# Optimization experiments

Hardware: AMD Instinct MI355X
Metric: run time of the kernel (lower is better)

Reference implementation:

```python
import jax, jax.numpy as jnp
import numpy as np

DIM = 1024
SRC_DIM = 1152
NUM_HEADS = 16
HEAD_DIM = DIM // NUM_HEADS  # 64
ROPE_BASE = 10000.0


def rope_tables(seq_len, head_dim):
    # matches RotaryPositionEmbedding: inv_freq over even indices, emb = cat([freqs, freqs])
    inv_freq = 1.0 / (ROPE_BASE ** (jnp.arange(0, head_dim, 2, dtype=jnp.float32) / head_dim))
    t = jnp.arange(seq_len, dtype=jnp.float32)
    freqs = t[:, None] * inv_freq[None, :]          # (L, D/2)
    emb = jnp.concatenate([freqs, freqs], axis=-1)  # (L, D)
    return jnp.cos(emb), jnp.sin(emb)


def rotate_half(x):
    # interleaved rotation as in the torch code
    x1 = x[..., ::2]
    x2 = x[..., 1::2]
    return jnp.stack((-x2, x1), axis=-1).reshape(x.shape)


def apply_rope(t, cos, sin):
    # t: (B, H, L, D); cos/sin: (L, D)
    return t * cos[None, None] + rotate_half(t) * sin[None, None]


def setup_inputs() -> dict:
    key = jax.random.key(0)
    ks = jax.random.split(key, 10)
    B, T, K = 2, 2048, 2048
    s_q = 1.0 / np.sqrt(DIM)
    s_kv = 1.0 / np.sqrt(SRC_DIM)
    return {
        "x": jax.random.normal(ks[0], (B, T, DIM), jnp.float32),
        "context": jax.random.normal(ks[1], (B, K, SRC_DIM), jnp.float32),
        "Wq": jax.random.normal(ks[2], (DIM, DIM), jnp.float32) * s_q,
        "bq": jnp.zeros((DIM,), jnp.float32),
        "Wk": jax.random.normal(ks[3], (DIM, SRC_DIM), jnp.float32) * s_kv,
        "bk": jnp.zeros((DIM,), jnp.float32),
        "Wv": jax.random.normal(ks[4], (DIM, SRC_DIM), jnp.float32) * s_kv,
        "bv": jnp.zeros((DIM,), jnp.float32),
        "Wo": jax.random.normal(ks[5], (DIM, DIM), jnp.float32) * s_q,
        "bo": jnp.zeros((DIM,), jnp.float32),
    }


def reference(x, context, Wq, bq, Wk, bk, Wv, bv, Wo, bo):
    B, T, C = x.shape
    K = context.shape[1]
    H, D = NUM_HEADS, HEAD_DIM

    q = x @ Wq.T + bq                 # (B, T, C)
    k = context @ Wk.T + bk           # (B, K, C)
    v = context @ Wv.T + bv           # (B, K, C)

    q = q.reshape(B, T, H, D).transpose(0, 2, 1, 3)  # (B, H, T, D)
    k = k.reshape(B, K, H, D).transpose(0, 2, 1, 3)  # (B, H, K, D)
    v = v.reshape(B, K, H, D).transpose(0, 2, 1, 3)

    cos_q, sin_q = rope_tables(T, D)
    cos_k, sin_k = rope_tables(K, D)
    q = apply_rope(q, cos_q, sin_q)
    k = apply_rope(k, cos_k, sin_k)

    scale = 1.0 / np.sqrt(D).astype(np.float32)
    scores = jnp.einsum('bhtd,bhkd->bhtk', q, k) * scale  # (B, H, T, K)
    weights = jax.nn.softmax(scores, axis=-1)
    out = jnp.einsum('bhtk,bhkd->bhtd', weights, v)        # (B, H, T, D)
    out = out.transpose(0, 2, 1, 3).reshape(B, T, C)
    return out @ Wo.T + bo
```

## Files before the change

### kernel.cpp

```cpp
#include <hip/hip_runtime.h>
#include <hip/hip_bf16.h>
#include <stdint.h>

typedef unsigned short u16;
typedef __attribute__((ext_vector_type(8))) short bf16x8;
typedef __attribute__((ext_vector_type(8))) unsigned short u16x8;
typedef __attribute__((ext_vector_type(4))) float f32x4;

#define BM 128
#define BN 128
#define BK 32
#define QBK 64
#define QSCALE 0.18033688f

__device__ __forceinline__ u16 f2bf(float f) {
    union { float f; uint32_t u; } v; v.f = f;
    uint32_t r = v.u + 0x7FFFu + ((v.u >> 16) & 1u);
    return (u16)(r >> 16);
}

__device__ __forceinline__ uint32_t cvt_pk_bf16(float lo, float hi) {
    uint32_t r;
    asm("v_cvt_pk_bf16_f32 %0, %1, %2" : "=v"(r) : "v"(lo), "v"(hi));
    return r;
}

__device__ __forceinline__ float fexp2(float x) {
    float r;
    asm volatile("v_exp_f32 %0, %1\n\ts_nop 0" : "=v"(r) : "v"(x));
    return r;
}

__device__ __forceinline__ void gload_lds16(const void* g, void* l) {
    __builtin_amdgcn_global_load_lds(
        (const __attribute__((address_space(1))) void*)(g),
        (__attribute__((address_space(3))) void*)(l),
        16, 0, 0);
}

__global__ void prep_kernel(const float* __restrict__ x, const float* __restrict__ ctx,
                            const float* __restrict__ Wq, const float* __restrict__ Wk,
                            const float* __restrict__ Wv, const float* __restrict__ Wo,
                            u16* __restrict__ xb, u16* __restrict__ cb,
                            u16* __restrict__ wqb, u16* __restrict__ wkb,
                            u16* __restrict__ wvb, u16* __restrict__ wob,
                            float2* __restrict__ cs) {
    int t = blockIdx.x * 256 + threadIdx.x;
    if (t < 3342336) {
        const float* src; u16* dst; int base;
        if      (t < 1048576) { src = x;   dst = xb;  base = 0; }
        else if (t < 2228224) { src = ctx; dst = cb;  base = 1048576; }
        else if (t < 2490368) { src = Wq;  dst = wqb; base = 2228224; }
        else if (t < 2785280) { src = Wk;  dst = wkb; base = 2490368; }
        else if (t < 3080192) { src = Wv;  dst = wvb; base = 2785280; }
        else                  { src = Wo;  dst = wob; base = 3080192; }
        int i = (t - base) * 4;
        float4 v = *reinterpret_cast<const float4*>(src + i);
        ushort4 o = { f2bf(v.x), f2bf(v.y), f2bf(v.z), f2bf(v.w) };
        *reinterpret_cast<ushort4*>(dst + i) = o;
    } else {
        int idx = t - 3342336;
        int tt = idx >> 5, j = idx & 31;
        float invf = 1.0f / powf(10000.0f, (float)(2 * j) / 64.0f);
        float ang = (float)tt * invf;
        cs[idx] = make_float2(cosf(ang), sinf(ang));
    }
}

__global__ __launch_bounds__(256, 3)
void qkv_gemm(const u16* __restrict__ xb, const u16* __restrict__ cb,
              const u16* __restrict__ wqb, const u16* __restrict__ wkb,
              const u16* __restrict__ wvb,
              const float* __restrict__ bq, const float* __restrict__ bk,
              const float* __restrict__ bv,
              u16* __restrict__ qo, u16* __restrict__ ko, u16* __restrict__ vo,
              const float2* __restrict__ cs)
{
    __shared__ __align__(16) u16 As[BM * QBK];
    __shared__ __align__(16) u16 Bs[BN * QBK];
    const int bid = blockIdx.x;
    const int wg = (bid & 7) * 96 + (bid >> 3);
    const int seg = wg >> 8, inner = wg & 255;
    const u16* A; const u16* Bm; const float* bias; u16* C;
    int N, K, mbase, nbase, rope, brow;
    float oscale;
    if (seg == 0)      { A = xb;  Bm = wqb; bias = bq; C = qo; N = 1024; K = 1024; rope = 1; brow = 0; oscale = QSCALE; nbase = (inner & 7) * BN;  mbase = (inner >> 3) * BM; }
    else if (seg == 1) { A = cb;  Bm = wkb; bias = bk; C = ko; N = 1024; K = 1152; rope = 1; brow = 0; oscale = 1.0f;   nbase = (inner & 7) * BN;  mbase = (inner >> 3) * BM; }
    else               { A = wvb; Bm = cb;  bias = bv; C = vo; N = 4096; K = 1152; rope = 0; brow = 1; oscale = 1.0f;   nbase = (inner & 31) * BN; mbase = (inner >> 5) * BM; }

    const int tid = threadIdx.x;
    const int wid = tid >> 6, lane = tid & 63;
    const int wr = wid >> 1, wc = wid & 1;
    const int l15 = lane & 15, l4 = lane >> 4;
    const int r8 = lane >> 3;
    const int cp = lane & 7;
    const int cl = cp ^ r8;

    f32x4 acc[4][4];
#pragma unroll
    for (int i = 0; i < 4; i++)
#pragma unroll
        for (int j = 0; j < 4; j++) acc[i][j] = (f32x4){0.f, 0.f, 0.f, 0.f};

    for (int k0 = 0; k0 < K; k0 += QBK) {
#pragma unroll
        for (int q = 0; q < 4; ++q) {
            int sg = wid * 4 + q;
            int row = sg * 8 + r8;
            gload_lds16(A  + (size_t)(mbase + row) * K + k0 + cl * 8, (void*)(As + sg * 512));
            gload_lds16(Bm + (size_t)(nbase + row) * K + k0 + cl * 8, (void*)(Bs + sg * 512));
        }
        __syncthreads();
        bf16x8 af[2][4], bfv[2][4];
#pragma unroll
        for (int kk = 0; kk < 2; kk++) {
#pragma unroll
            for (int i = 0; i < 4; i++) {
                int r = wr * 64 + i * 16 + l15;
                af[kk][i] = *(const bf16x8*)(As + r * 64 + (((kk * 4 + l4) ^ (r & 7)) * 8));
            }
#pragma unroll
            for (int j = 0; j < 4; j++) {
                int r = wc * 64 + j * 16 + l15;
                bfv[kk][j] = *(const bf16x8*)(Bs + r * 64 + (((kk * 4 + l4) ^ (r & 7)) * 8));
            }
        }
        __builtin_amdgcn_s_setprio(1);
#pragma unroll
        for (int kk = 0; kk < 2; kk++)
#pragma unroll
            for (int i = 0; i < 4; i++)
#pragma unroll
                for (int j = 0; j < 4; j++)
                    acc[i][j] = __builtin_amdgcn_mfma_f32_16x16x32_bf16(af[kk][i], bfv[kk][j], acc[i][j], 0, 0, 0);
        __builtin_amdgcn_s_setprio(0);
        __syncthreads();
    }

#pragma unroll
    for (int i = 0; i < 4; i++) {
#pragma unroll
        for (int j = 0; j < 4; j++) {
#pragma unroll
            for (int r = 0; r < 4; r++) {
                int row = mbase + wr * 64 + i * 16 + l4 * 4 + r;
                int col = nbase + wc * 64 + j * 16 + l15;
                float v = acc[i][j][r] + (brow ? bias[row] : bias[col]);
                if (rope) {
                    float part = __shfl_xor(v, 1);
                    float2 c2 = cs[(row & 2047) * 32 + (col & 31)];
                    v = v * c2.x + ((col & 1) ? part * c2.y : -part * c2.y);
                    v *= oscale;
                }
                C[(size_t)row * N + col] = f2bf(v);
            }
        }
    }
}

__global__ __launch_bounds__(256, 2)
void gemm_out(const u16* __restrict__ A, const u16* __restrict__ B,
              const float* __restrict__ bias, float* __restrict__ C,
              int M, int N, int K)
{
    __shared__ __align__(16) u16 As[BM * QBK];
    __shared__ __align__(16) u16 Bs[64 * QBK];
    const int tid = threadIdx.x;
    const int wid = tid >> 6, lane = tid & 63;
    const int wr = wid >> 1, wc = wid & 1;
    const int l15 = lane & 15, l4 = lane >> 4;
    const int mbase = blockIdx.y * BM, nbase = blockIdx.x * 64;
    const int r8 = lane >> 3;
    const int cp = lane & 7;
    const int cl = cp ^ r8;

    f32x4 acc[4][2];
#pragma unroll
    for (int i = 0; i < 4; i++)
#pragma unroll
        for (int j = 0; j < 2; j++) acc[i][j] = (f32x4){0.f, 0.f, 0.f, 0.f};

    for (int k0 = 0; k0 < K; k0 += QBK) {
#pragma unroll
        for (int q = 0; q < 4; ++q) {
            int sg = wid * 4 + q;
            int row = sg * 8 + r8;
            gload_lds16(A + (size_t)(mbase + row) * K + k0 + cl * 8, (void*)(As + sg * 512));
        }
        {
            int sg = wid * 2 + (lane >> 5);
        }
#pragma unroll
        for (int q = 0; q < 2; ++q) {
            int sg = wid * 2 + q;
            int row = sg * 8 + r8;
            gload_lds16(B + (size_t)(nbase + row) * K + k0 + cl * 8, (void*)(Bs + sg * 512));
        }
        __syncthreads();
        bf16x8 af[2][4], bfv[2][2];
#pragma unroll
        for (int kk = 0; kk < 2; kk++) {
#pragma unroll
            for (int i = 0; i < 4; i++) {
                int r = wr * 64 + i * 16 + l15;
                af[kk][i] = *(const bf16x8*)(As + r * 64 + (((kk * 4 + l4) ^ (r & 7)) * 8));
            }
#pragma unroll
            for (int j = 0; j < 2; j++) {
                int r = wc * 32 + j * 16 + l15;
                bfv[kk][j] = *(const bf16x8*)(Bs + r * 64 + (((kk * 4 + l4) ^ (r & 7)) * 8));
            }
        }
        __builtin_amdgcn_s_setprio(1);
#pragma unroll
        for (int kk = 0; kk < 2; kk++)
#pragma unroll
            for (int i = 0; i < 4; i++)
#pragma unroll
                for (int j = 0; j < 2; j++)
                    acc[i][j] = __builtin_amdgcn_mfma_f32_16x16x32_bf16(af[kk][i], bfv[kk][j], acc[i][j], 0, 0, 0);
        __builtin_amdgcn_s_setprio(0);
        __syncthreads();
    }

#pragma unroll
    for (int i = 0; i < 4; i++)
#pragma unroll
        for (int j = 0; j < 2; j++)
#pragma unroll
            for (int r = 0; r < 4; r++) {
                int row = mbase + wr * 64 + i * 16 + l4 * 4 + r;
                int col = nbase + wc * 32 + j * 16 + l15;
                C[(size_t)row * N + col] = acc[i][j][r] + bias[col];
            }
}

__device__ __forceinline__ int invrow(int R) {
    return 32 * (R >> 5) + 8 * ((R >> 2) & 3) + 4 * ((R >> 4) & 1) + (R & 3);
}

__global__ __launch_bounds__(512, 4)
void attn_kernel(const u16* __restrict__ Qb, const u16* __restrict__ Kb,
                 const u16* __restrict__ VT, u16* __restrict__ Ob)
{
    const int qt = blockIdx.x;
    const int bh = blockIdx.y;
    const int b = bh >> 4, h = bh & 15;
    __shared__ __align__(16) u16 Ks[2][4096];
    __shared__ __align__(16) u16 Vs[2][4096];
    const int tid = threadIdx.x, wv = tid >> 6, lane = tid & 63;
    const int l15 = lane & 15, l4 = lane >> 4;

    const int r8 = lane >> 3;
    const int cp = lane & 7;
    const int cl = cp ^ r8;
    const int RK = wv * 8 + r8;
    const u16* ksrc = Kb + (size_t)(b * 2048 + invrow(RK)) * 1024 + h * 64 + cl * 8;
    const u16* vsrc = VT + (size_t)(h * 64 + RK) * 4096 + b * 2048 + cl * 8;

    const u16* qrow = Qb + (size_t)(b * 2048 + qt * 128 + wv * 16 + l15) * 1024 + h * 64;
    bf16x8 qf0 = *(const bf16x8*)(qrow + l4 * 8);
    bf16x8 qf1 = *(const bf16x8*)(qrow + 32 + l4 * 8);

    const int swz = l15 & 7;
    const int q0o = (l4 ^ swz) * 8;
    const int q1o = ((4 + l4) ^ swz) * 8;

    f32x4 accO[4];
    float denom = 0.f;
#pragma unroll
    for (int i = 0; i < 4; i++) accO[i] = (f32x4){0.f, 0.f, 0.f, 0.f};

    auto stageK = [&](int bs, int kt) {
        gload_lds16(ksrc + (size_t)kt * 65536, (void*)&Ks[bs][wv * 512]);
    };
    auto stageV = [&](int bs, int kt) {
        gload_lds16(vsrc + kt * 64, (void*)&Vs[bs][wv * 512]);
    };

    stageK(0, 0);
    __syncthreads();

    f32x4 sA[4], sB[4];

    auto finish_tile = [&](f32x4 (&sold)[4], int vbuf) {
        float p[4][4];
        float rs = 0.f;
#pragma unroll
        for (int j = 0; j < 4; j++)
#pragma unroll
            for (int r = 0; r < 4; r++) {
                p[j][r] = fexp2(sold[j][r]);
                rs += p[j][r];
            }
        rs += __shfl_xor(rs, 16);
        rs += __shfl_xor(rs, 32);
        denom += rs;
        union { uint32_t u[4]; bf16x8 v; } B0u, B1u;
        B0u.u[0] = cvt_pk_bf16(p[0][0], p[0][1]);
        B0u.u[1] = cvt_pk_bf16(p[0][2], p[0][3]);
        B0u.u[2] = cvt_pk_bf16(p[1][0], p[1][1]);
        B0u.u[3] = cvt_pk_bf16(p[1][2], p[1][3]);
        B1u.u[0] = cvt_pk_bf16(p[2][0], p[2][1]);
        B1u.u[1] = cvt_pk_bf16(p[2][2], p[2][3]);
        B1u.u[2] = cvt_pk_bf16(p[3][0], p[3][1]);
        B1u.u[3] = cvt_pk_bf16(p[3][2], p[3][3]);
        __builtin_amdgcn_s_setprio(1);
#pragma unroll
        for (int i = 0; i < 4; i++) {
            const u16* vp = &Vs[vbuf][(i * 16 + l15) * 64];
            bf16x8 v0 = *(const bf16x8*)(vp + q0o);
            bf16x8 v1 = *(const bf16x8*)(vp + q1o);
            accO[i] = __builtin_amdgcn_mfma_f32_16x16x32_bf16(v0, B0u.v, accO[i], 0, 0, 0);
            accO[i] = __builtin_amdgcn_mfma_f32_16x16x32_bf16(v1, B1u.v, accO[i], 0, 0, 0);
        }
        __builtin_amdgcn_s_setprio(0);
    };

    auto body = [&](int kt, f32x4 (&snew)[4], f32x4 (&sold)[4]) {
        const int kb = kt & 1;
#pragma unroll
        for (int j = 0; j < 4; j++) snew[j] = (f32x4){0.f, 0.f, 0.f, 0.f};
        __builtin_amdgcn_s_setprio(1);
#pragma unroll
        for (int j = 0; j < 4; j++) {
            const u16* rp = &Ks[kb][(j * 16 + l15) * 64];
            bf16x8 a0 = *(const bf16x8*)(rp + q0o);
            bf16x8 a1 = *(const bf16x8*)(rp + q1o);
            snew[j] = __builtin_amdgcn_mfma_f32_16x16x32_bf16(a0, qf0, snew[j], 0, 0, 0);
            snew[j] = __builtin_amdgcn_mfma_f32_16x16x32_bf16(a1, qf1, snew[j], 0, 0, 0);
        }
        __builtin_amdgcn_s_setprio(0);
        if (kt < 31) stageK(kb ^ 1, kt + 1);
        stageV(kb ^ 1, kt);
        if (kt > 0) finish_tile(sold, kb);
        __syncthreads();
    };

    for (int kt2 = 0; kt2 < 32; kt2 += 2) {
        body(kt2, sA, sB);
        body(kt2 + 1, sB, sA);
    }
    finish_tile(sB, 0);

    float rd = 1.0f / denom;
    u16* orow = Ob + (size_t)(b * 2048 + qt * 128 + wv * 16 + l15) * 1024 + h * 64;
#pragma unroll
    for (int i = 0; i < 4; i++) {
        uint2 st;
        st.x = cvt_pk_bf16(accO[i][0] * rd, accO[i][1] * rd);
        st.y = cvt_pk_bf16(accO[i][2] * rd, accO[i][3] * rd);
        *(uint2*)(orow + i * 16 + l4 * 4) = st;
    }
}

extern "C" void kernel_launch(void* const* d_in, const int* in_sizes, int n_in,
                              void* d_out, int out_size, void* d_ws, size_t ws_size,
                              hipStream_t stream) {
    const float* x   = (const float*)d_in[0];
    const float* ctx = (const float*)d_in[1];
    const float* Wq  = (const float*)d_in[2];
    const float* bq  = (const float*)d_in[3];
    const float* Wk  = (const float*)d_in[4];
    const float* bk  = (const float*)d_in[5];
    const float* Wv  = (const float*)d_in[6];
    const float* bv  = (const float*)d_in[7];
    const float* Wo  = (const float*)d_in[8];
    const float* bo  = (const float*)d_in[9];
    float* out = (float*)d_out;

    char* ws = (char*)d_ws;
    size_t off = 0;
    auto alloc = [&](size_t bytes) { void* p = ws + off; off += (bytes + 255) & ~255ULL; return p; };
    u16* x_bf  = (u16*)alloc(4096ULL * 1024 * 2);
    u16* c_bf  = (u16*)alloc(4096ULL * 1152 * 2);
    u16* wq_bf = (u16*)alloc(1024ULL * 1024 * 2);
    u16* wk_bf = (u16*)alloc(1024ULL * 1152 * 2);
    u16* wv_bf = (u16*)alloc(1024ULL * 1152 * 2);
    u16* wo_bf = (u16*)alloc(1024ULL * 1024 * 2);
    float2* cs = (float2*)alloc(2048ULL * 32 * 8);
    u16* q_bf  = (u16*)alloc(4096ULL * 1024 * 2);
    u16* k_bf  = (u16*)alloc(4096ULL * 1024 * 2);
    u16* vT    = (u16*)alloc(1024ULL * 4096 * 2);
    u16* a_bf  = (u16*)alloc(4096ULL * 1024 * 2);

    prep_kernel<<<13312, 256, 0, stream>>>(x, ctx, Wq, Wk, Wv, Wo,
                                           x_bf, c_bf, wq_bf, wk_bf, wv_bf, wo_bf, cs);
    qkv_gemm<<<768, 256, 0, stream>>>(x_bf, c_bf, wq_bf, wk_bf, wv_bf,
                                      bq, bk, bv, q_bf, k_bf, vT, cs);
    attn_kernel<<<dim3(16, 32), 512, 0, stream>>>(q_bf, k_bf, vT, a_bf);
    gemm_out<<<dim3(16, 32), 256, 0, stream>>>(a_bf, wo_bf, bo, out, 4096, 1024, 1024);
}
```

Measured before the change: 125.9 us.

## Process two KV tiles per barrier with four-slot K/V LDS ring

The attention loop now handles two key tiles per iteration, with K and V staged into a four-slot LDS ring instead of a double buffer. This halves the number of __syncthreads barriers and gives more independent MFMA work between them. In exchange LDS use doubles, launch bounds drop from 4 to 2 blocks per CU, and more score registers are live, so occupancy falls. A dead leftover block in the projection GEMM is also removed.

```diff
diff --git a/kernel.cpp b/kernel.cpp
--- a/kernel.cpp
+++ b/kernel.cpp
@@ -187,9 +187,6 @@
             int row = sg * 8 + r8;
             gload_lds16(A + (size_t)(mbase + row) * K + k0 + cl * 8, (void*)(As + sg * 512));
         }
-        {
-            int sg = wid * 2 + (lane >> 5);
-        }
 #pragma unroll
         for (int q = 0; q < 2; ++q) {
             int sg = wid * 2 + q;
@@ -239,15 +236,15 @@
     return 32 * (R >> 5) + 8 * ((R >> 2) & 3) + 4 * ((R >> 4) & 1) + (R & 3);
 }
 
-__global__ __launch_bounds__(512, 4)
+__global__ __launch_bounds__(512, 2)
 void attn_kernel(const u16* __restrict__ Qb, const u16* __restrict__ Kb,
                  const u16* __restrict__ VT, u16* __restrict__ Ob)
 {
     const int qt = blockIdx.x;
     const int bh = blockIdx.y;
     const int b = bh >> 4, h = bh & 15;
-    __shared__ __align__(16) u16 Ks[2][4096];
-    __shared__ __align__(16) u16 Vs[2][4096];
+    __shared__ __align__(16) u16 Ks[4][4096];
+    __shared__ __align__(16) u16 Vs[4][4096];
     const int tid = threadIdx.x, wv = tid >> 6, lane = tid & 63;
     const int l15 = lane & 15, l4 = lane >> 4;
 
@@ -271,19 +268,36 @@
 #pragma unroll
     for (int i = 0; i < 4; i++) accO[i] = (f32x4){0.f, 0.f, 0.f, 0.f};
 
-    auto stageK = [&](int bs, int kt) {
-        gload_lds16(ksrc + (size_t)kt * 65536, (void*)&Ks[bs][wv * 512]);
+    auto stageK = [&](int slot, int kt) {
+        gload_lds16(ksrc + (size_t)kt * 65536, (void*)&Ks[slot][wv * 512]);
     };
-    auto stageV = [&](int bs, int kt) {
-        gload_lds16(vsrc + kt * 64, (void*)&Vs[bs][wv * 512]);
+    auto stageV = [&](int slot, int kt) {
+        gload_lds16(vsrc + kt * 64, (void*)&Vs[slot][wv * 512]);
     };
 
     stageK(0, 0);
+    stageK(1, 1);
     __syncthreads();
 
-    f32x4 sA[4], sB[4];
-
-    auto finish_tile = [&](f32x4 (&sold)[4], int vbuf) {
+    f32x4 sA0[4], sA1[4], sB0[4], sB1[4];
+
+    auto qk = [&](int kt, f32x4 (&s)[4]) {
+#pragma unroll
+        for (int j = 0; j < 4; j++) s[j] = (f32x4){0.f, 0.f, 0.f, 0.f};
+        const int slot = kt & 3;
+        __builtin_amdgcn_s_setprio(1);
+#pragma unroll
+        for (int j = 0; j < 4; j++) {
+            const u16* rp = &Ks[slot][(j * 16 + l15) * 64];
+            bf16x8 a0 = *(const bf16x8*)(rp + q0o);
+            bf16x8 a1 = *(const bf16x8*)(rp + q1o);
+            s[j] = __builtin_amdgcn_mfma_f32_16x16x32_bf16(a0, qf0, s[j], 0, 0, 0);
+            s[j] = __builtin_amdgcn_mfma_f32_16x16x32_bf16(a1, qf1, s[j], 0, 0, 0);
+        }
+        __builtin_amdgcn_s_setprio(0);
+    };
+
+    auto finish_tile = [&](f32x4 (&sold)[4], int vslot) {
         float p[4][4];
         float rs = 0.f;
 #pragma unroll
@@ -308,7 +322,7 @@
         __builtin_amdgcn_s_setprio(1);
 #pragma unroll
         for (int i = 0; i < 4; i++) {
-            const u16* vp = &Vs[vbuf][(i * 16 + l15) * 64];
+            const u16* vp = &Vs[vslot][(i * 16 + l15) * 64];
             bf16x8 v0 = *(const bf16x8*)(vp + q0o);
             bf16x8 v1 = *(const bf16x8*)(vp + q1o);
             accO[i] = __builtin_amdgcn_mfma_f32_16x16x32_bf16(v0, B0u.v, accO[i], 0, 0, 0);
@@ -317,31 +331,28 @@
         __builtin_amdgcn_s_setprio(0);
     };
 
-    auto body = [&](int kt, f32x4 (&snew)[4], f32x4 (&sold)[4]) {
-        const int kb = kt & 1;
-#pragma unroll
-        for (int j = 0; j < 4; j++) snew[j] = (f32x4){0.f, 0.f, 0.f, 0.f};
-        __builtin_amdgcn_s_setprio(1);
-#pragma unroll
-        for (int j = 0; j < 4; j++) {
-            const u16* rp = &Ks[kb][(j * 16 + l15) * 64];
-            bf16x8 a0 = *(const bf16x8*)(rp + q0o);
-            bf16x8 a1 = *(const bf16x8*)(rp + q1o);
-            snew[j] = __builtin_amdgcn_mfma_f32_16x16x32_bf16(a0, qf0, snew[j], 0, 0, 0);
-            snew[j] = __builtin_amdgcn_mfma_f32_16x16x32_bf16(a1, qf1, snew[j], 0, 0, 0);
-        }
-        __builtin_amdgcn_s_setprio(0);
-        if (kt < 31) stageK(kb ^ 1, kt + 1);
-        stageV(kb ^ 1, kt);
-        if (kt > 0) finish_tile(sold, kb);
+    auto pairbody = [&](int ip, f32x4 (&n0)[4], f32x4 (&n1)[4],
+                        f32x4 (&o0)[4], f32x4 (&o1)[4]) {
+        const int t0 = 2 * ip, t1 = t0 + 1;
+        qk(t0, n0);
+        qk(t1, n1);
+        if (t0 + 2 < 32) stageK((t0 + 2) & 3, t0 + 2);
+        if (t1 + 2 < 32) stageK((t1 + 2) & 3, t1 + 2);
+        stageV(t0 & 3, t0);
+        stageV(t1 & 3, t1);
+        if (ip > 0) {
+            finish_tile(o0, (t0 - 2) & 3);
+            finish_tile(o1, (t1 - 2) & 3);
+        }
         __syncthreads();
     };
 
-    for (int kt2 = 0; kt2 < 32; kt2 += 2) {
-        body(kt2, sA, sB);
-        body(kt2 + 1, sB, sA);
-    }
-    finish_tile(sB, 0);
+    for (int ip2 = 0; ip2 < 16; ip2 += 2) {
+        pairbody(ip2, sA0, sA1, sB0, sB1);
+        pairbody(ip2 + 1, sB0, sB1, sA0, sA1);
+    }
+    finish_tile(sB0, 30 & 3);
+    finish_tile(sB1, 31 & 3);
 
     float rd = 1.0f / denom;
     u16* orow = Ob + (size_t)(b * 2048 + qt * 128 + wv * 16 + l15) * 1024 + h * 64;
```

New measurement: 132.6 us. +5.3%, slower.
